# Performance work log

Hardware: AMD Instinct MI355X
Metric: run time of the kernel (lower is better)

The kernel has to match this reference:

```python
import jax, jax.numpy as jnp
import numpy as np

N, IN_C, HID, H1, E, EP = 4096, 256, 128, 4, 131072, 131072
TH, TL, FF = 4, 2, 512  # transformer heads, layers, ffn dim
D = HID  # transformer d_model


def setup_inputs() -> dict:
    key = jax.random.key(0)
    ks = jax.random.split(key, 32)
    s = 0.05
    inp = {
        'features': jax.random.normal(ks[0], (N, IN_C), jnp.float32),
        'src': jax.random.randint(ks[1], (E,), 0, N),
        'dst': jax.random.randint(ks[2], (E,), 0, N),
        'psrc': jax.random.randint(ks[3], (EP,), 0, N),
        'pdst': jax.random.randint(ks[4], (EP,), 0, N),
        # GAT layer 1: in=256 -> heads=4, out=128
        'W1': jax.random.normal(ks[5], (H1 * HID, IN_C), jnp.float32) * s,
        'al1': jax.random.normal(ks[6], (H1, HID), jnp.float32) * s,
        'ar1': jax.random.normal(ks[7], (H1, HID), jnp.float32) * s,
        'b1': jnp.zeros((H1 * HID,), jnp.float32),
        # GAT layer 2: in=512 -> heads=1, out=128
        'W2': jax.random.normal(ks[8], (HID, H1 * HID), jnp.float32) * s,
        'al2': jax.random.normal(ks[9], (1, HID), jnp.float32) * s,
        'ar2': jax.random.normal(ks[10], (1, HID), jnp.float32) * s,
        'b2': jnp.zeros((HID,), jnp.float32),
        # Transformer encoder (TL layers, torch TransformerEncoderLayer post-norm, relu)
        'tw_qkv': jax.random.normal(ks[11], (TL, 3 * D, D), jnp.float32) * s,
        'tb_qkv': jnp.zeros((TL, 3 * D), jnp.float32),
        'tw_o': jax.random.normal(ks[12], (TL, D, D), jnp.float32) * s,
        'tb_o': jnp.zeros((TL, D), jnp.float32),
        'ln1_g': jnp.ones((TL, D), jnp.float32),
        'ln1_b': jnp.zeros((TL, D), jnp.float32),
        'tw_ff1': jax.random.normal(ks[13], (TL, FF, D), jnp.float32) * s,
        'tb_ff1': jnp.zeros((TL, FF), jnp.float32),
        'tw_ff2': jax.random.normal(ks[14], (TL, D, FF), jnp.float32) * s,
        'tb_ff2': jnp.zeros((TL, D), jnp.float32),
        'ln2_g': jnp.ones((TL, D), jnp.float32),
        'ln2_b': jnp.zeros((TL, D), jnp.float32),
        # decoder MLP
        'fc1_w': jax.random.normal(ks[15], (HID, 2 * HID), jnp.float32) * s,
        'fc1_b': jnp.zeros((HID,), jnp.float32),
        'fc2_w': jax.random.normal(ks[16], (1, HID), jnp.float32) * s,
        'fc2_b': jnp.zeros((1,), jnp.float32),
    }
    return inp


def _leaky(x):
    return jnp.where(x > 0, x, 0.2 * x)


def _gat(x, W, al, ar, b, src, dst, n):
    H, F = al.shape
    h = (x @ W.T).reshape(n, H, F)  # [N,H,F]
    el = jnp.sum(h * al[None], -1)  # [N,H]
    er = jnp.sum(h * ar[None], -1)
    e = _leaky(el[src] + er[dst])  # [E,H]
    m = jax.ops.segment_max(e, dst, num_segments=n)
    ex = jnp.exp(e - m[dst])
    ssum = jax.ops.segment_sum(ex, dst, num_segments=n)
    alpha = ex / ssum[dst]  # edge softmax over incoming edges of dst
    out = jax.ops.segment_sum(h[src] * alpha[:, :, None], dst, num_segments=n)
    return out + b.reshape(1, H, F)


def _ln(x, g, b):
    mu = jnp.mean(x, -1, keepdims=True)
    var = jnp.mean((x - mu) ** 2, -1, keepdims=True)
    return (x - mu) / jnp.sqrt(var + 1e-5) * g + b


def _encoder_layer(h, wqkv, bqkv, wo, bo, g1, b1, wf1, bf1, wf2, bf2, g2, b2):
    n, d = h.shape
    hd = d // TH
    qkv = h @ wqkv.T + bqkv
    q, k, v = jnp.split(qkv, 3, axis=-1)
    q = q.reshape(n, TH, hd)
    k = k.reshape(n, TH, hd)
    v = v.reshape(n, TH, hd)
    scores = jnp.einsum('qhd,khd->hqk', q, k) / jnp.sqrt(jnp.float32(hd))
    attn = jax.nn.softmax(scores, axis=-1)
    o = jnp.einsum('hqk,khd->qhd', attn, v).reshape(n, d) @ wo.T + bo
    h = _ln(h + o, g1, b1)
    ff = jax.nn.relu(h @ wf1.T + bf1) @ wf2.T + bf2
    return _ln(h + ff, g2, b2)


def reference(features, W1, al1, ar1, b1, W2, al2, ar2, b2,
              tw_qkv, tb_qkv, tw_o, tb_o, ln1_g, ln1_b,
              tw_ff1, tb_ff1, tw_ff2, tb_ff2, ln2_g, ln2_b,
              fc1_w, fc1_b, fc2_w, fc2_b, src, dst, psrc, pdst):
    n = features.shape[0]
    h = _gat(features, W1, al1, ar1, b1, src, dst, n)  # [N,4,128]
    h = jax.nn.relu(h.reshape(n, -1))                  # [N,512]
    h = _gat(h, W2, al2, ar2, b2, src, dst, n)[:, 0]   # [N,128]
    for i in range(TL):
        h = _encoder_layer(h, tw_qkv[i], tb_qkv[i], tw_o[i], tb_o[i],
                           ln1_g[i], ln1_b[i], tw_ff1[i], tb_ff1[i],
                           tw_ff2[i], tb_ff2[i], ln2_g[i], ln2_b[i])
    ef = jnp.concatenate([h[psrc], h[pdst]], axis=1)   # [EP,256]
    x = jax.nn.relu(ef @ fc1_w.T + fc1_b)
    return jax.nn.sigmoid(x @ fc2_w.T + fc2_b)         # [EP,1]
```

## Files before the change

kernel.cpp:

```cpp
#include <hip/hip_runtime.h>
#include <hip/hip_bf16.h>
#include <math.h>

#define NN   4096
#define INC  256
#define HIDF 128
#define H1H  4
#define DM   128
#define THD  4
#define FFD  512

typedef __attribute__((ext_vector_type(8))) short bf16x8;
typedef __attribute__((ext_vector_type(4))) float f32x4;

__device__ __forceinline__ float leaky(float x){ return x > 0.f ? x : 0.2f*x; }

__device__ __forceinline__ ushort f2b(float f){
  __hip_bfloat16 h = __float2bfloat16(f);
  return __builtin_bit_cast(ushort, h);
}
__device__ __forceinline__ unsigned pk2(float a, float b){
  return (unsigned)f2b(a) | ((unsigned)f2b(b) << 16);
}
__device__ __forceinline__ float b2f(unsigned u){ return __uint_as_float(u << 16); }
__device__ __forceinline__ float b2flo(unsigned u){ return __uint_as_float(u << 16); }
__device__ __forceinline__ float b2fhi(unsigned u){ return __uint_as_float(u & 0xffff0000u); }

__device__ __forceinline__ int kvperm(int kv){
  return (kv & ~31) | ((kv & 12) << 1) | ((kv >> 2) & 4) | (kv & 3);
}

template<bool BIAS, bool RELU, bool OUTBF, bool ABF>
__global__ __launch_bounds__(256) void gemm_mf(
    const void* __restrict__ Av, const ushort* __restrict__ Wb,
    const float* __restrict__ bias, void* __restrict__ Cv,
    int M, int N, int K, int ldw)
{
  __shared__ uint4 As4[512];
  __shared__ uint4 Bs4[512];
  int tid = threadIdx.x;
  int row0 = blockIdx.y * 64, col0 = blockIdx.x * 64;
  int wid = tid >> 6, lane = tid & 63;
  int wm = wid >> 1, wn = wid & 1;
  int ql = lane & 15, g = lane >> 4;
  const f32x4 z4 = {0.f,0.f,0.f,0.f};
  f32x4 acc[2][2] = {z4,z4,z4,z4};

  for (int k0 = 0; k0 < K; k0 += 64) {
    #pragma unroll
    for (int p = 0; p < 2; p++) {
      int idx = tid + p*256;
      int ko = idx & 7, mm = idx >> 3;
      if constexpr (ABF) {
        As4[ko*64 + mm] = *(const uint4*)((const ushort*)Av + (size_t)(row0 + mm)*K + k0 + ko*8);
      } else {
        const float* sa = (const float*)Av + (size_t)(row0 + mm)*K + k0 + ko*8;
        float4 a0 = *(const float4*)sa;
        float4 a1 = *(const float4*)(sa + 4);
        uint4 av;
        av.x = pk2(a0.x, a0.y); av.y = pk2(a0.z, a0.w);
        av.z = pk2(a1.x, a1.y); av.w = pk2(a1.z, a1.w);
        As4[ko*64 + mm] = av;
      }
      Bs4[ko*64 + mm] = *(const uint4*)(Wb + (size_t)(col0 + mm)*ldw + k0 + ko*8);
    }
    __syncthreads();
    #pragma unroll
    for (int kk = 0; kk < 2; kk++) {
      int ko = kk*4 + g;
      bf16x8 a0 = *((const bf16x8*)As4 + ko*64 + wm*32 + ql);
      bf16x8 a1 = *((const bf16x8*)As4 + ko*64 + wm*32 + 16 + ql);
      bf16x8 b0 = *((const bf16x8*)Bs4 + ko*64 + wn*32 + ql);
      bf16x8 b1 = *((const bf16x8*)Bs4 + ko*64 + wn*32 + 16 + ql);
      acc[0][0] = __builtin_amdgcn_mfma_f32_16x16x32_bf16(a0, b0, acc[0][0], 0,0,0);
      acc[0][1] = __builtin_amdgcn_mfma_f32_16x16x32_bf16(a0, b1, acc[0][1], 0,0,0);
      acc[1][0] = __builtin_amdgcn_mfma_f32_16x16x32_bf16(a1, b0, acc[1][0], 0,0,0);
      acc[1][1] = __builtin_amdgcn_mfma_f32_16x16x32_bf16(a1, b1, acc[1][1], 0,0,0);
    }
    __syncthreads();
  }
  float bvs[2] = {0.f, 0.f};
  if (BIAS) {
    bvs[0] = bias[col0 + wn*32 + ql];
    bvs[1] = bias[col0 + wn*32 + 16 + ql];
  }
  #pragma unroll
  for (int fm = 0; fm < 2; fm++)
    #pragma unroll
    for (int fn = 0; fn < 2; fn++) {
      int row = row0 + wm*32 + fm*16 + g*4;
      int col = col0 + wn*32 + fn*16 + ql;
      #pragma unroll
      for (int r = 0; r < 4; r++) {
        float v = acc[fm][fn][r];
        if (BIAS) v += bvs[fn];
        if (RELU) v = fmaxf(v, 0.f);
        if (OUTBF) ((ushort*)Cv)[(size_t)(row + r)*N + col] = f2b(v);
        else       ((float*)Cv)[(size_t)(row + r)*N + col] = v;
      }
    }
}

__global__ __launch_bounds__(256) void gemm_qkv(
    const ushort* __restrict__ Ab, const ushort* __restrict__ Wb,
    const float* __restrict__ bias,
    ushort* __restrict__ qb, ushort* __restrict__ kt, ushort* __restrict__ vt)
{
  __shared__ uint4 As4[512];
  __shared__ uint4 Bs4[512];
  int tid = threadIdx.x;
  int row0 = blockIdx.y * 64, col0 = blockIdx.x * 64;
  int wid = tid >> 6, lane = tid & 63;
  int wm = wid >> 1, wn = wid & 1;
  int ql = lane & 15, g = lane >> 4;
  const f32x4 z4 = {0.f,0.f,0.f,0.f};
  f32x4 acc[2][2] = {z4,z4,z4,z4};

  for (int k0 = 0; k0 < 128; k0 += 64) {
    #pragma unroll
    for (int p = 0; p < 2; p++) {
      int idx = tid + p*256;
      int ko = idx & 7, mm = idx >> 3;
      As4[ko*64 + mm] = *(const uint4*)(Ab + (size_t)(row0 + mm)*128 + k0 + ko*8);
      Bs4[ko*64 + mm] = *(const uint4*)(Wb + (size_t)(col0 + mm)*128 + k0 + ko*8);
    }
    __syncthreads();
    #pragma unroll
    for (int kk = 0; kk < 2; kk++) {
      int ko = kk*4 + g;
      bf16x8 a0 = *((const bf16x8*)As4 + ko*64 + wm*32 + ql);
      bf16x8 a1 = *((const bf16x8*)As4 + ko*64 + wm*32 + 16 + ql);
      bf16x8 b0 = *((const bf16x8*)Bs4 + ko*64 + wn*32 + ql);
      bf16x8 b1 = *((const bf16x8*)Bs4 + ko*64 + wn*32 + 16 + ql);
      acc[0][0] = __builtin_amdgcn_mfma_f32_16x16x32_bf16(a0, b0, acc[0][0], 0,0,0);
      acc[0][1] = __builtin_amdgcn_mfma_f32_16x16x32_bf16(a0, b1, acc[0][1], 0,0,0);
      acc[1][0] = __builtin_amdgcn_mfma_f32_16x16x32_bf16(a1, b0, acc[1][0], 0,0,0);
      acc[1][1] = __builtin_amdgcn_mfma_f32_16x16x32_bf16(a1, b1, acc[1][1], 0,0,0);
    }
    __syncthreads();
  }
  float bvs[2];
  bvs[0] = bias[col0 + wn*32 + ql];
  bvs[1] = bias[col0 + wn*32 + 16 + ql];
  #pragma unroll
  for (int fm = 0; fm < 2; fm++)
    #pragma unroll
    for (int fn = 0; fn < 2; fn++) {
      int row = row0 + wm*32 + fm*16 + g*4;
      int col = col0 + wn*32 + fn*16 + ql;
      #pragma unroll
      for (int r = 0; r < 4; r++) {
        float v = acc[fm][fn][r] + bvs[fn];
        int kv = row + r;
        if (col < 128) {
          qb[(size_t)kv*128 + col] = f2b(v * 0.25505654708f);
        } else if (col < 256) {
          int hh = (col - 128) >> 5, d = (col - 128) & 31;
          kt[(size_t)hh*131072 + (size_t)kv*32 + d] = f2b(v);
        } else {
          int hh = (col - 256) >> 5, d = (col - 256) & 31;
          vt[(size_t)hh*131072 + (size_t)(kv >> 5)*1024 + (d >> 4)*512
             + (d & 15)*32 + kvperm(kv & 31)] = f2b(v);
        }
      }
    }
}

__global__ __launch_bounds__(256) void gemm_ln(
    const ushort* __restrict__ Ab, const ushort* __restrict__ Wb,
    const float* __restrict__ bias, ushort* __restrict__ h,
    const float* __restrict__ lng, const float* __restrict__ lnb, int K)
{
  __shared__ uint4 As4[128];
  __shared__ uint4 Bs4[1024];
  __shared__ float xs[16][132];
  int tid = threadIdx.x;
  int row0 = blockIdx.x * 16;
  int wv = tid >> 6, lane = tid & 63;
  int ql = lane & 15, g = lane >> 4;
  const f32x4 z4 = {0.f,0.f,0.f,0.f};
  f32x4 acc[2] = {z4, z4};

  for (int k0 = 0; k0 < K; k0 += 64) {
    if (tid < 128) {
      int ko = tid & 7, mm = tid >> 3;
      As4[ko*16 + mm] = *(const uint4*)(Ab + (size_t)(row0 + mm)*K + k0 + ko*8);
    }
    #pragma unroll
    for (int p = 0; p < 4; p++) {
      int idx = tid + p*256;
      int ko = idx & 7, nn = idx >> 3;
      Bs4[ko*128 + nn] = *(const uint4*)(Wb + (size_t)nn*K + k0 + ko*8);
    }
    __syncthreads();
    #pragma unroll
    for (int kk = 0; kk < 2; kk++) {
      int ko = kk*4 + g;
      bf16x8 a = *((const bf16x8*)As4 + ko*16 + ql);
      #pragma unroll
      for (int fn = 0; fn < 2; fn++) {
        bf16x8 b = *((const bf16x8*)Bs4 + ko*128 + wv*32 + fn*16 + ql);
        acc[fn] = __builtin_amdgcn_mfma_f32_16x16x32_bf16(a, b, acc[fn], 0,0,0);
      }
    }
    __syncthreads();
  }
  #pragma unroll
  for (int fn = 0; fn < 2; fn++) {
    int col = wv*32 + fn*16 + ql;
    float bv = bias[col];
    #pragma unroll
    for (int r = 0; r < 4; r++) xs[g*4 + r][col] = acc[fn][r] + bv;
  }
  __syncthreads();
  int rl = tid >> 4, cl = tid & 15, c0 = cl * 8;
  ushort* hrow = h + (size_t)(row0 + rl)*128;
  uint4 rv = *(const uint4*)(hrow + c0);
  float x[8];
  x[0] = xs[rl][c0+0] + b2flo(rv.x); x[1] = xs[rl][c0+1] + b2fhi(rv.x);
  x[2] = xs[rl][c0+2] + b2flo(rv.y); x[3] = xs[rl][c0+3] + b2fhi(rv.y);
  x[4] = xs[rl][c0+4] + b2flo(rv.z); x[5] = xs[rl][c0+5] + b2fhi(rv.z);
  x[6] = xs[rl][c0+6] + b2flo(rv.w); x[7] = xs[rl][c0+7] + b2fhi(rv.w);
  float s1 = 0.f, s2 = 0.f;
  #pragma unroll
  for (int i = 0; i < 8; i++) { s1 += x[i]; s2 += x[i]*x[i]; }
  #pragma unroll
  for (int st = 1; st < 16; st <<= 1) {
    s1 += __shfl_xor(s1, st); s2 += __shfl_xor(s2, st);
  }
  float mean = s1 * (1.f/128.f);
  float var  = s2 * (1.f/128.f) - mean*mean;
  float rstd = rsqrtf(var + 1e-5f);
  float o[8];
  #pragma unroll
  for (int i = 0; i < 8; i += 4) {
    float4 g4 = *(const float4*)(lng + c0 + i);
    float4 b4 = *(const float4*)(lnb + c0 + i);
    o[i+0] = (x[i+0]-mean)*rstd*g4.x + b4.x;
    o[i+1] = (x[i+1]-mean)*rstd*g4.y + b4.y;
    o[i+2] = (x[i+2]-mean)*rstd*g4.z + b4.z;
    o[i+3] = (x[i+3]-mean)*rstd*g4.w + b4.w;
  }
  uint4 ov; ov.x = pk2(o[0],o[1]); ov.y = pk2(o[2],o[3]);
  ov.z = pk2(o[4],o[5]); ov.w = pk2(o[6],o[7]);
  *(uint4*)(hrow + c0) = ov;
}

__global__ __launch_bounds__(256) void cvt_weights(
    const float* __restrict__ W1, const float* __restrict__ W2,
    const float* __restrict__ qkv, const float* __restrict__ o,
    const float* __restrict__ ff1, const float* __restrict__ ff2,
    const float* __restrict__ fc1, const float* __restrict__ fc1b,
    ushort* __restrict__ out, float* __restrict__ bias256)
{
  if (blockIdx.x == 608) {
    int t = threadIdx.x;
    bias256[t] = (t < 128) ? fc1b[t] : 0.f;
    return;
  }
  int i4 = (blockIdx.x*256 + threadIdx.x) * 4;
  const float* s; int loc;
  size_t dst = i4;
  if      (i4 < 131072) { s = W1;  loc = i4; }
  else if (i4 < 196608) { s = W2;  loc = i4 - 131072; }
  else if (i4 < 294912) { s = qkv; loc = i4 - 196608; }
  else if (i4 < 327680) { s = o;   loc = i4 - 294912; }
  else if (i4 < 458752) { s = ff1; loc = i4 - 327680; }
  else if (i4 < 589824) { s = ff2; loc = i4 - 458752; }
  else {
    s = fc1; loc = i4 - 589824;
    int j = loc >> 8, k2 = loc & 255;
    dst = 589824 + ((k2 >= 128) ? 16384 : 0) + j*128 + (k2 & 127);
  }
  float4 v = *(const float4*)(s + loc);
  uint2 w; w.x = pk2(v.x, v.y); w.y = pk2(v.z, v.w);
  *(uint2*)(out + dst) = w;
}

__global__ void zero_kernel(int* p, int n) {
  int i = blockIdx.x * blockDim.x + threadIdx.x;
  if (i < n) p[i] = 0;
}
__global__ void count_kernel(const int* __restrict__ dst, int* __restrict__ deg, int E) {
  int e = blockIdx.x * blockDim.x + threadIdx.x;
  if (e < E) atomicAdd(&deg[dst[e]], 1);
}
__global__ __launch_bounds__(1024) void scan_kernel(
    const int* __restrict__ deg, int* __restrict__ rowstart, int* __restrict__ cursor)
{
  __shared__ int sdata[1024];
  int t = threadIdx.x;
  int base = t * 4;
  int v0 = deg[base], v1 = deg[base+1], v2 = deg[base+2], v3 = deg[base+3];
  int tot = v0 + v1 + v2 + v3;
  sdata[t] = tot;
  __syncthreads();
  for (int off = 1; off < 1024; off <<= 1) {
    int x = (t >= off) ? sdata[t - off] : 0;
    __syncthreads();
    sdata[t] += x;
    __syncthreads();
  }
  int run = sdata[t] - tot;
  rowstart[base]   = run; cursor[base]   = run; run += v0;
  rowstart[base+1] = run; cursor[base+1] = run; run += v1;
  rowstart[base+2] = run; cursor[base+2] = run; run += v2;
  rowstart[base+3] = run; cursor[base+3] = run; run += v3;
  if (t == 1023) rowstart[4096] = run;
}
__global__ void fill_kernel(const int* __restrict__ src, const int* __restrict__ dst,
                            int* __restrict__ cursor, int* __restrict__ nbr, int E) {
  int e = blockIdx.x * blockDim.x + threadIdx.x;
  if (e < E) {
    int p = atomicAdd(&cursor[dst[e]], 1);
    nbr[p] = src[e];
  }
}

template<int H>
__global__ __launch_bounds__(256) void elr_kernel(
    const ushort* __restrict__ hmat, const float* __restrict__ al,
    const float* __restrict__ ar, float* __restrict__ el, float* __restrict__ er)
{
  int w = threadIdx.x >> 6, lane = threadIdx.x & 63;
  int n = blockIdx.x * 4 + w;
  if constexpr (H == 4) {
    int hh = lane >> 4, f0 = (lane & 15) * 8;
    bf16x8 hv = *(const bf16x8*)(hmat + (size_t)n*512 + hh*128 + f0);
    float4 a0 = *(const float4*)(al + hh*128 + f0);
    float4 a1 = *(const float4*)(al + hh*128 + f0 + 4);
    float4 r0 = *(const float4*)(ar + hh*128 + f0);
    float4 r1 = *(const float4*)(ar + hh*128 + f0 + 4);
    float x[8];
    #pragma unroll
    for (int i = 0; i < 8; i++) x[i] = b2f((ushort)hv[i]);
    float e1 = x[0]*a0.x + x[1]*a0.y + x[2]*a0.z + x[3]*a0.w
             + x[4]*a1.x + x[5]*a1.y + x[6]*a1.z + x[7]*a1.w;
    float e2 = x[0]*r0.x + x[1]*r0.y + x[2]*r0.z + x[3]*r0.w
             + x[4]*r1.x + x[5]*r1.y + x[6]*r1.z + x[7]*r1.w;
    #pragma unroll
    for (int s = 1; s < 16; s <<= 1) { e1 += __shfl_xor(e1, s); e2 += __shfl_xor(e2, s); }
    if ((lane & 15) == 0) { el[n*4 + hh] = e1; er[n*4 + hh] = e2; }
  } else {
    int f0 = lane * 2;
    unsigned u = *(const unsigned*)(hmat + (size_t)n*128 + f0);
    float x0 = b2flo(u), x1 = b2fhi(u);
    float2 av = *(const float2*)(al + f0);
    float2 rv = *(const float2*)(ar + f0);
    float e1 = x0*av.x + x1*av.y;
    float e2 = x0*rv.x + x1*rv.y;
    #pragma unroll
    for (int s = 1; s < 64; s <<= 1) { e1 += __shfl_xor(e1, s); e2 += __shfl_xor(e2, s); }
    if (lane == 0) { el[n] = e1; er[n] = e2; }
  }
}

__global__ __launch_bounds__(256) void gat_agg4(
    const ushort* __restrict__ hsrc, const float* __restrict__ el, const float* __restrict__ er,
    const int* __restrict__ rowstart, const int* __restrict__ nbr,
    const float* __restrict__ bias, ushort* __restrict__ out)
{
  __shared__ float s_alpha[4][256][4];
  __shared__ int   s_nbr[4][256];
  int wv = threadIdx.x >> 6, lane = threadIdx.x & 63;
  int n = blockIdx.x * 4 + wv;
  int e0 = rowstart[n];
  int deg = rowstart[n+1] - e0;
  float4 ern = *(const float4*)(er + (size_t)n*4);
  int hh = lane >> 4;
  float acc[8] = {};
  if (deg > 0 && deg <= 256) {
    float se0=0.f, se1=0.f, se2=0.f, se3=0.f;
    for (int i = lane; i < deg; i += 64) {
      int s = nbr[e0 + i];
      s_nbr[wv][i] = s;
      float4 ev = *(const float4*)(el + (size_t)s*4);
      float p0 = __expf(leaky(ev.x + ern.x));
      float p1 = __expf(leaky(ev.y + ern.y));
      float p2 = __expf(leaky(ev.z + ern.z));
      float p3 = __expf(leaky(ev.w + ern.w));
      s_alpha[wv][i][0] = p0; s_alpha[wv][i][1] = p1;
      s_alpha[wv][i][2] = p2; s_alpha[wv][i][3] = p3;
      se0 += p0; se1 += p1; se2 += p2; se3 += p3;
    }
    #pragma unroll
    for (int st = 1; st < 64; st <<= 1) {
      se0 += __shfl_xor(se0, st); se1 += __shfl_xor(se1, st);
      se2 += __shfl_xor(se2, st); se3 += __shfl_xor(se3, st);
    }
    float si = 1.f / ((hh == 0) ? se0 : (hh == 1) ? se1 : (hh == 2) ? se2 : se3);
    #pragma unroll 4
    for (int i = 0; i < deg; i++) {
      float a = s_alpha[wv][i][hh] * si;
      int s = s_nbr[wv][i];
      uint4 hv = *(const uint4*)(hsrc + (size_t)s*512 + lane*8);
      acc[0] += a * b2flo(hv.x); acc[1] += a * b2fhi(hv.x);
      acc[2] += a * b2flo(hv.y); acc[3] += a * b2fhi(hv.y);
      acc[4] += a * b2flo(hv.z); acc[5] += a * b2fhi(hv.z);
      acc[6] += a * b2flo(hv.w); acc[7] += a * b2fhi(hv.w);
    }
  } else if (deg > 0) {
    float se0=0.f, se1=0.f, se2=0.f, se3=0.f;
    for (int i = lane; i < deg; i += 64) {
      int s = nbr[e0 + i];
      float4 ev = *(const float4*)(el + (size_t)s*4);
      se0 += __expf(leaky(ev.x + ern.x));
      se1 += __expf(leaky(ev.y + ern.y));
      se2 += __expf(leaky(ev.z + ern.z));
      se3 += __expf(leaky(ev.w + ern.w));
    }
    #pragma unroll
    for (int st = 1; st < 64; st <<= 1) {
      se0 += __shfl_xor(se0, st); se1 += __shfl_xor(se1, st);
      se2 += __shfl_xor(se2, st); se3 += __shfl_xor(se3, st);
    }
    float si0 = 1.f/se0, si1 = 1.f/se1, si2 = 1.f/se2, si3 = 1.f/se3;
    for (int c = 0; c < deg; c += 256) {
      int cn = min(256, deg - c);
      for (int i = lane; i < cn; i += 64) {
        int s = nbr[e0 + c + i];
        s_nbr[wv][i] = s;
        float4 ev = *(const float4*)(el + (size_t)s*4);
        s_alpha[wv][i][0] = __expf(leaky(ev.x + ern.x)) * si0;
        s_alpha[wv][i][1] = __expf(leaky(ev.y + ern.y)) * si1;
        s_alpha[wv][i][2] = __expf(leaky(ev.z + ern.z)) * si2;
        s_alpha[wv][i][3] = __expf(leaky(ev.w + ern.w)) * si3;
      }
      #pragma unroll 4
      for (int i = 0; i < cn; i++) {
        float a = s_alpha[wv][i][hh];
        int s = s_nbr[wv][i];
        uint4 hv = *(const uint4*)(hsrc + (size_t)s*512 + lane*8);
        acc[0] += a * b2flo(hv.x); acc[1] += a * b2fhi(hv.x);
        acc[2] += a * b2flo(hv.y); acc[3] += a * b2fhi(hv.y);
        acc[4] += a * b2flo(hv.z); acc[5] += a * b2fhi(hv.z);
        acc[6] += a * b2flo(hv.w); acc[7] += a * b2fhi(hv.w);
      }
    }
  }
  const float* bp = bias + lane*8;
  float4 b0 = *(const float4*)(bp);
  float4 b1 = *(const float4*)(bp + 4);
  float v0 = fmaxf(acc[0]+b0.x, 0.f), v1 = fmaxf(acc[1]+b0.y, 0.f);
  float v2 = fmaxf(acc[2]+b0.z, 0.f), v3 = fmaxf(acc[3]+b0.w, 0.f);
  float v4 = fmaxf(acc[4]+b1.x, 0.f), v5 = fmaxf(acc[5]+b1.y, 0.f);
  float v6 = fmaxf(acc[6]+b1.z, 0.f), v7 = fmaxf(acc[7]+b1.w, 0.f);
  uint4 ov; ov.x = pk2(v0,v1); ov.y = pk2(v2,v3); ov.z = pk2(v4,v5); ov.w = pk2(v6,v7);
  *(uint4*)(out + (size_t)n*512 + lane*8) = ov;
}

__global__ __launch_bounds__(256) void gat_agg1(
    const ushort* __restrict__ hsrc, const float* __restrict__ el, const float* __restrict__ er,
    const int* __restrict__ rowstart, const int* __restrict__ nbr,
    const float* __restrict__ bias, ushort* __restrict__ out)
{
  __shared__ float s_alpha[4][256];
  __shared__ int   s_nbr[4][256];
  int wv = threadIdx.x >> 6, lane = threadIdx.x & 63;
  int n = blockIdx.x * 4 + wv;
  int e0 = rowstart[n];
  int deg = rowstart[n+1] - e0;
  float ern = er[n];
  float a0 = 0.f, a1 = 0.f;
  if (deg > 0 && deg <= 256) {
    float se = 0.f;
    for (int i = lane; i < deg; i += 64) {
      int s = nbr[e0 + i];
      s_nbr[wv][i] = s;
      float p = __expf(leaky(el[s] + ern));
      s_alpha[wv][i] = p;
      se += p;
    }
    #pragma unroll
    for (int st = 1; st < 64; st <<= 1) se += __shfl_xor(se, st);
    float si = 1.f / se;
    #pragma unroll 4
    for (int i = 0; i < deg; i++) {
      float a = s_alpha[wv][i] * si;
      int s = s_nbr[wv][i];
      unsigned u = *(const unsigned*)(hsrc + (size_t)s*128 + lane*2);
      a0 += a * b2flo(u);
      a1 += a * b2fhi(u);
    }
  } else if (deg > 0) {
    float se = 0.f;
    for (int i = lane; i < deg; i += 64)
      se += __expf(leaky(el[nbr[e0 + i]] + ern));
    #pragma unroll
    for (int st = 1; st < 64; st <<= 1) se += __shfl_xor(se, st);
    float si = 1.f / se;
    for (int c = 0; c < deg; c += 256) {
      int cn = min(256, deg - c);
      for (int i = lane; i < cn; i += 64) {
        int s = nbr[e0 + c + i];
        s_nbr[wv][i] = s;
        s_alpha[wv][i] = __expf(leaky(el[s] + ern)) * si;
      }
      #pragma unroll 4
      for (int i = 0; i < cn; i++) {
        float a = s_alpha[wv][i];
        int s = s_nbr[wv][i];
        unsigned u = *(const unsigned*)(hsrc + (size_t)s*128 + lane*2);
        a0 += a * b2flo(u);
        a1 += a * b2fhi(u);
      }
    }
    a0 *= si; a1 *= si;
    a0 /= si; a1 /= si;
  }
  float v0 = a0 + bias[lane*2], v1 = a1 + bias[lane*2 + 1];
  *(unsigned*)(out + (size_t)n*128 + lane*2) = pk2(v0, v1);
}

#define LOADFRAGS(KF, VF, KV)                                              \
  {                                                                        \
    int _kv = (KV);                                                        \
    if (_kv < 1024) {                                                      \
      const ushort* _kp = kptr + (size_t)_kv * 32;                         \
      const ushort* _vp = vptr + (size_t)_kv * 32;                         \
      KF[0] = *(const bf16x8*)(_kp);                                       \
      KF[1] = *(const bf16x8*)(_kp + 512);                                 \
      KF[2] = *(const bf16x8*)(_kp + 1024);                                \
      KF[3] = *(const bf16x8*)(_kp + 1536);                                \
      VF[0] = *(const bf16x8*)(_vp);                                       \
      VF[1] = *(const bf16x8*)(_vp + 1024);                                \
      VF[2] = *(const bf16x8*)(_vp + 512);                                 \
      VF[3] = *(const bf16x8*)(_vp + 1536);                                \
    }                                                                      \
  }

#define QPASS(QF, LS, OA, OB, KF, VF)                                      \
  {                                                                        \
    f32x4 st0 = __builtin_amdgcn_mfma_f32_16x16x32_bf16(KF[0], QF, z4, 0, 0, 0); \
    f32x4 st1 = __builtin_amdgcn_mfma_f32_16x16x32_bf16(KF[1], QF, z4, 0, 0, 0); \
    f32x4 st2 = __builtin_amdgcn_mfma_f32_16x16x32_bf16(KF[2], QF, z4, 0, 0, 0); \
    f32x4 st3 = __builtin_amdgcn_mfma_f32_16x16x32_bf16(KF[3], QF, z4, 0, 0, 0); \
    float pvv[16];                                                         \
    _Pragma("unroll")                                                      \
    for (int i = 0; i < 4; i++) {                                          \
      pvv[i] = st0[i]; pvv[4+i] = st1[i]; pvv[8+i] = st2[i]; pvv[12+i] = st3[i]; \
    }                                                                      \
    _Pragma("unroll")                                                      \
    for (int i = 0; i < 16; i++) { pvv[i] = exp2f(pvv[i]); LS += pvv[i]; } \
    bf16x8 pf0 = { (short)f2b(pvv[0]),  (short)f2b(pvv[1]),  (short)f2b(pvv[2]),  (short)f2b(pvv[3]),   \
                   (short)f2b(pvv[4]),  (short)f2b(pvv[5]),  (short)f2b(pvv[6]),  (short)f2b(pvv[7]) }; \
    bf16x8 pf1 = { (short)f2b(pvv[8]),  (short)f2b(pvv[9]),  (short)f2b(pvv[10]), (short)f2b(pvv[11]),  \
                   (short)f2b(pvv[12]), (short)f2b(pvv[13]), (short)f2b(pvv[14]), (short)f2b(pvv[15]) };\
    OA = __builtin_amdgcn_mfma_f32_16x16x32_bf16(VF[0], pf0, OA, 0, 0, 0); \
    OA = __builtin_amdgcn_mfma_f32_16x16x32_bf16(VF[1], pf1, OA, 0, 0, 0); \
    OB = __builtin_amdgcn_mfma_f32_16x16x32_bf16(VF[2], pf0, OB, 0, 0, 0); \
    OB = __builtin_amdgcn_mfma_f32_16x16x32_bf16(VF[3], pf1, OB, 0, 0, 0); \
  }

#define ATTN_BODY(KF, VF, KN, VN, KV)                                      \
  {                                                                        \
    LOADFRAGS(KN, VN, (KV) + 64);                                          \
    QPASS(qf0, ls0, o00, o01, KF, VF);                                     \
    QPASS(qf1, ls1, o10, o11, KF, VF);                                     \
  }

__global__ __launch_bounds__(256) void attn_mfma(
    const ushort* __restrict__ qb,
    const ushort* __restrict__ kt,
    const ushort* __restrict__ vt,
    ushort* __restrict__ attnout)
{
  int lane = threadIdx.x & 63;
  int w    = threadIdx.x >> 6;
  int head = blockIdx.x >> 7;
  int q0   = (blockIdx.x & 127) * 32;
  int ql = lane & 15;
  int g  = lane >> 4;
  const f32x4 z4 = {0.f, 0.f, 0.f, 0.f};
  int kvbase = w * 1024;

  bf16x8 qf0 = *(const bf16x8*)(qb + (size_t)(q0 + ql)*128      + head*32 + g*8);
  bf16x8 qf1 = *(const bf16x8*)(qb + (size_t)(q0 + 16 + ql)*128 + head*32 + g*8);
  const ushort* kptr = kt + (size_t)head*131072 + (size_t)kvbase*32 + ql*32 + g*8;
  const ushort* vptr = vt + (size_t)head*131072 + (size_t)kvbase*32 + ql*32 + g*8;

  float ls0 = 0.f, ls1 = 0.f;
  f32x4 o00 = z4, o01 = z4, o10 = z4, o11 = z4;

  bf16x8 kfA[4], vfA[4], kfB[4], vfB[4];
  LOADFRAGS(kfA, vfA, 0);
  for (int kv0 = 0; kv0 < 1024; kv0 += 128) {
    ATTN_BODY(kfA, vfA, kfB, vfB, kv0);
    ATTN_BODY(kfB, vfB, kfA, vfA, kv0 + 64);
  }

  ls0 += __shfl_xor(ls0, 16); ls0 += __shfl_xor(ls0, 32);
  ls1 += __shfl_xor(ls1, 16); ls1 += __shfl_xor(ls1, 32);

  __shared__ float so[4][32][36];
  __shared__ float sl[4][32];
  if (g == 0) { sl[w][ql] = ls0; sl[w][16 + ql] = ls1; }
  #pragma unroll
  for (int r = 0; r < 4; r++) {
    so[w][ql][g*4 + r]           = o00[r];
    so[w][ql][16 + g*4 + r]      = o01[r];
    so[w][16 + ql][g*4 + r]      = o10[r];
    so[w][16 + ql][16 + g*4 + r] = o11[r];
  }
  __syncthreads();
  int q  = threadIdx.x >> 3;
  int d0 = (threadIdx.x & 7) * 4;
  float L = 0.f, O0 = 0.f, O1 = 0.f, O2 = 0.f, O3 = 0.f;
  #pragma unroll
  for (int w2 = 0; w2 < 4; w2++) {
    L  += sl[w2][q];
    O0 += so[w2][q][d0];
    O1 += so[w2][q][d0+1];
    O2 += so[w2][q][d0+2];
    O3 += so[w2][q][d0+3];
  }
  float rl = 1.f / L;
  uint2 w2v; w2v.x = pk2(O0*rl, O1*rl); w2v.y = pk2(O2*rl, O3*rl);
  *(uint2*)(attnout + (size_t)(q0 + q)*128 + head*32 + d0) = w2v;
}

__global__ __launch_bounds__(256) void pair_kernel(
    const ushort* __restrict__ ABp,
    const int* __restrict__ ps, const int* __restrict__ pd,
    const float* __restrict__ fc2w, const float* __restrict__ fc2b,
    float* __restrict__ out, int EP)
{
  int gw = (blockIdx.x * blockDim.x + threadIdx.x) >> 6;
  int lane = threadIdx.x & 63;
  int nw = (gridDim.x * blockDim.x) >> 6;
  float w0 = fc2w[2*lane], w1 = fc2w[2*lane + 1];
  float bb = fc2b[0];
  for (int p = gw; p < EP; p += nw) {
    int s = ps[p], d = pd[p];
    unsigned av = *(const unsigned*)(ABp + (size_t)s*256 + 2*lane);
    unsigned bv = *(const unsigned*)(ABp + (size_t)d*256 + 128 + 2*lane);
    float a0 = b2flo(av), a1 = b2fhi(av);
    float b0 = b2flo(bv), b1 = b2fhi(bv);
    float acc = fmaxf(a0 + b0, 0.f)*w0 + fmaxf(a1 + b1, 0.f)*w1;
    #pragma unroll
    for (int off = 32; off > 0; off >>= 1) acc += __shfl_down(acc, off);
    if (lane == 0) out[p] = 1.f / (1.f + __expf(-(acc + bb)));
  }
}

extern "C" void kernel_launch(void* const* d_in, const int* in_sizes, int n_in,
                              void* d_out, int out_size, void* d_ws, size_t ws_size,
                              hipStream_t stream)
{
  const float* features = (const float*)d_in[0];
  const int*   src      = (const int*)d_in[1];
  const int*   dst      = (const int*)d_in[2];
  const int*   psrc     = (const int*)d_in[3];
  const int*   pdst     = (const int*)d_in[4];
  const float* W1   = (const float*)d_in[5];
  const float* al1  = (const float*)d_in[6];
  const float* ar1  = (const float*)d_in[7];
  const float* b1   = (const float*)d_in[8];
  const float* W2   = (const float*)d_in[9];
  const float* al2  = (const float*)d_in[10];
  const float* ar2  = (const float*)d_in[11];
  const float* b2   = (const float*)d_in[12];
  const float* tw_qkv = (const float*)d_in[13];
  const float* tb_qkv = (const float*)d_in[14];
  const float* tw_o   = (const float*)d_in[15];
  const float* tb_o   = (const float*)d_in[16];
  const float* ln1_g  = (const float*)d_in[17];
  const float* ln1_b  = (const float*)d_in[18];
  const float* tw_ff1 = (const float*)d_in[19];
  const float* tb_ff1 = (const float*)d_in[20];
  const float* tw_ff2 = (const float*)d_in[21];
  const float* tb_ff2 = (const float*)d_in[22];
  const float* ln2_g  = (const float*)d_in[23];
  const float* ln2_b  = (const float*)d_in[24];
  const float* fc1_w  = (const float*)d_in[25];
  const float* fc1_b  = (const float*)d_in[26];
  const float* fc2_w  = (const float*)d_in[27];
  const float* fc2_b  = (const float*)d_in[28];
  int E  = in_sizes[1];
  int EP = in_sizes[3];

  float* ws = (float*)d_ws;
  size_t off = 0;
  auto alloc = [&](size_t n) { float* p = ws + off; off += n; return p; };
  ushort* hb    = (ushort*)alloc((size_t)NN * 64);
  ushort* h1b   = (ushort*)alloc((size_t)NN * 256);
  ushort* h2b   = (ushort*)alloc((size_t)NN * 256);
  ushort* bigb  = (ushort*)alloc((size_t)NN * 256);
  ushort* hgb   = (ushort*)alloc((size_t)NN * 64);
  ushort* qb    = (ushort*)alloc((size_t)NN * 64);
  ushort* attnb = (ushort*)alloc((size_t)NN * 64);
  ushort* kt    = (ushort*)alloc((size_t)NN * 64);
  ushort* vt    = (ushort*)alloc((size_t)NN * 64);
  ushort* wbf   = (ushort*)alloc(622592/2);
  ushort* ABp   = (ushort*)alloc((size_t)NN * 128);
  float*  bias256 = alloc(256);
  float*  el1   = alloc((size_t)NN * 4);
  float*  er1   = alloc((size_t)NN * 4);
  float*  el2   = alloc((size_t)NN);
  float*  er2   = alloc((size_t)NN);
  int* ibase    = (int*)(ws + off);
  int* deg      = ibase;
  int* rowstart = ibase + 4096;
  int* cursor   = rowstart + 4097;
  int* nbr      = cursor + 4096;

  const size_t oW1 = 0, oW2 = 131072, oQKV = 196608, oO = 294912,
               oFF1 = 327680, oFF2 = 458752, oFC1 = 589824;

  cvt_weights<<<609, 256, 0, stream>>>(W1, W2, tw_qkv, tw_o, tw_ff1, tw_ff2,
                                       fc1_w, fc1_b, wbf, bias256);

  zero_kernel<<<16, 256, 0, stream>>>(deg, 4096);
  count_kernel<<<(E + 255)/256, 256, 0, stream>>>(dst, deg, E);
  scan_kernel<<<1, 1024, 0, stream>>>(deg, rowstart, cursor);
  fill_kernel<<<(E + 255)/256, 256, 0, stream>>>(src, dst, cursor, nbr, E);

  gemm_mf<false,false,true,false><<<dim3(8, 64), 256, 0, stream>>>(
      features, wbf + oW1, nullptr, h1b, NN, 512, 256, 256);
  elr_kernel<4><<<1024, 256, 0, stream>>>(h1b, al1, ar1, el1, er1);
  gat_agg4<<<1024, 256, 0, stream>>>(h1b, el1, er1, rowstart, nbr, b1, h2b);

  gemm_mf<false,false,true,true><<<dim3(2, 64), 256, 0, stream>>>(
      h2b, wbf + oW2, nullptr, hgb, NN, 128, 512, 512);
  elr_kernel<1><<<1024, 256, 0, stream>>>(hgb, al2, ar2, el2, er2);
  gat_agg1<<<1024, 256, 0, stream>>>(hgb, el2, er2, rowstart, nbr, b2, hb);

  for (int l = 0; l < 2; l++) {
    gemm_qkv<<<dim3(6, 64), 256, 0, stream>>>(
        hb, wbf + oQKV + (size_t)l*49152, tb_qkv + l*384, qb, kt, vt);
    attn_mfma<<<512, 256, 0, stream>>>(qb, kt, vt, attnb);
    gemm_ln<<<256, 256, 0, stream>>>(
        attnb, wbf + oO + (size_t)l*16384, tb_o + l*128, hb,
        ln1_g + l*128, ln1_b + l*128, 128);
    gemm_mf<true,true,true,true><<<dim3(8, 64), 256, 0, stream>>>(
        hb, wbf + oFF1 + (size_t)l*65536, tb_ff1 + l*512, bigb, NN, 512, 128, 128);
    gemm_ln<<<256, 256, 0, stream>>>(
        bigb, wbf + oFF2 + (size_t)l*65536, tb_ff2 + l*128, hb,
        ln2_g + l*128, ln2_b + l*128, 512);
  }

  gemm_mf<true,false,true,true><<<dim3(4, 64), 256, 0, stream>>>(
      hb, wbf + oFC1, bias256, ABp, NN, 256, 128, 128);
  pair_kernel<<<1024, 256, 0, stream>>>(ABp, psrc, pdst, fc2_w, fc2_b, (float*)d_out, EP);
}
```

Before: 218.8 us.

## Split attention KV across 8 waves, pre-convert features, batch pair pairs, memset degrees

The attention kernel now runs 512 threads per block, and each of 8 waves covers 512 keys instead of 4 waves covering 1024. This raises parallelism per block at the cost of a larger shared-memory reduction. Input features are converted to bf16 in a separate kernel so the first GEMM reads bf16 instead of fp32. The pair kernel processes two edges per wave iteration to overlap gathers. A redundant multiply/divide in gat_agg1 is removed, and the zero kernel is replaced with hipMemsetAsync.

```diff
diff --git a/kernel.cpp b/kernel.cpp
--- a/kernel.cpp
+++ b/kernel.cpp
@@ -277,10 +277,15 @@
   *(uint2*)(out + dst) = w;
 }
 
-__global__ void zero_kernel(int* p, int n) {
-  int i = blockIdx.x * blockDim.x + threadIdx.x;
-  if (i < n) p[i] = 0;
-}
+__global__ __launch_bounds__(256) void cvt_feat(
+    const float* __restrict__ f, ushort* __restrict__ o)
+{
+  int i = (blockIdx.x * 256 + threadIdx.x) * 4;
+  float4 v = *(const float4*)(f + i);
+  uint2 w; w.x = pk2(v.x, v.y); w.y = pk2(v.z, v.w);
+  *(uint2*)(o + i) = w;
+}
+
 __global__ void count_kernel(const int* __restrict__ dst, int* __restrict__ deg, int E) {
   int e = blockIdx.x * blockDim.x + threadIdx.x;
   if (e < E) atomicAdd(&deg[dst[e]], 1);
@@ -505,8 +510,6 @@
         a1 += a * b2fhi(u);
       }
     }
-    a0 *= si; a1 *= si;
-    a0 /= si; a1 /= si;
   }
   float v0 = a0 + bias[lane*2], v1 = a1 + bias[lane*2 + 1];
   *(unsigned*)(out + (size_t)n*128 + lane*2) = pk2(v0, v1);
@@ -515,7 +518,7 @@
 #define LOADFRAGS(KF, VF, KV)                                              \
   {                                                                        \
     int _kv = (KV);                                                        \
-    if (_kv < 1024) {                                                      \
+    if (_kv < 512) {                                                       \
       const ushort* _kp = kptr + (size_t)_kv * 32;                         \
       const ushort* _vp = vptr + (size_t)_kv * 32;                         \
       KF[0] = *(const bf16x8*)(_kp);                                       \
@@ -559,7 +562,7 @@
     QPASS(qf1, ls1, o10, o11, KF, VF);                                     \
   }
 
-__global__ __launch_bounds__(256) void attn_mfma(
+__global__ __launch_bounds__(512) void attn_mfma(
     const ushort* __restrict__ qb,
     const ushort* __restrict__ kt,
     const ushort* __restrict__ vt,
@@ -572,7 +575,7 @@
   int ql = lane & 15;
   int g  = lane >> 4;
   const f32x4 z4 = {0.f, 0.f, 0.f, 0.f};
-  int kvbase = w * 1024;
+  int kvbase = w * 512;
 
   bf16x8 qf0 = *(const bf16x8*)(qb + (size_t)(q0 + ql)*128      + head*32 + g*8);
   bf16x8 qf1 = *(const bf16x8*)(qb + (size_t)(q0 + 16 + ql)*128 + head*32 + g*8);
@@ -584,7 +587,7 @@
 
   bf16x8 kfA[4], vfA[4], kfB[4], vfB[4];
   LOADFRAGS(kfA, vfA, 0);
-  for (int kv0 = 0; kv0 < 1024; kv0 += 128) {
+  for (int kv0 = 0; kv0 < 512; kv0 += 128) {
     ATTN_BODY(kfA, vfA, kfB, vfB, kv0);
     ATTN_BODY(kfB, vfB, kfA, vfA, kv0 + 64);
   }
@@ -592,8 +595,8 @@
   ls0 += __shfl_xor(ls0, 16); ls0 += __shfl_xor(ls0, 32);
   ls1 += __shfl_xor(ls1, 16); ls1 += __shfl_xor(ls1, 32);
 
-  __shared__ float so[4][32][36];
-  __shared__ float sl[4][32];
+  __shared__ float so[8][32][36];
+  __shared__ float sl[8][32];
   if (g == 0) { sl[w][ql] = ls0; sl[w][16 + ql] = ls1; }
   #pragma unroll
   for (int r = 0; r < 4; r++) {
@@ -603,20 +606,17 @@
     so[w][16 + ql][16 + g*4 + r] = o11[r];
   }
   __syncthreads();
-  int q  = threadIdx.x >> 3;
-  int d0 = (threadIdx.x & 7) * 4;
-  float L = 0.f, O0 = 0.f, O1 = 0.f, O2 = 0.f, O3 = 0.f;
+  int q  = threadIdx.x >> 4;
+  int d0 = (threadIdx.x & 15) * 2;
+  float L = 0.f, O0 = 0.f, O1 = 0.f;
   #pragma unroll
-  for (int w2 = 0; w2 < 4; w2++) {
+  for (int w2 = 0; w2 < 8; w2++) {
     L  += sl[w2][q];
     O0 += so[w2][q][d0];
     O1 += so[w2][q][d0+1];
-    O2 += so[w2][q][d0+2];
-    O3 += so[w2][q][d0+3];
   }
   float rl = 1.f / L;
-  uint2 w2v; w2v.x = pk2(O0*rl, O1*rl); w2v.y = pk2(O2*rl, O3*rl);
-  *(uint2*)(attnout + (size_t)(q0 + q)*128 + head*32 + d0) = w2v;
+  *(unsigned*)(attnout + (size_t)(q0 + q)*128 + head*32 + d0) = pk2(O0*rl, O1*rl);
 }
 
 __global__ __launch_bounds__(256) void pair_kernel(
@@ -630,16 +630,28 @@
   int nw = (gridDim.x * blockDim.x) >> 6;
   float w0 = fc2w[2*lane], w1 = fc2w[2*lane + 1];
   float bb = fc2b[0];
-  for (int p = gw; p < EP; p += nw) {
-    int s = ps[p], d = pd[p];
-    unsigned av = *(const unsigned*)(ABp + (size_t)s*256 + 2*lane);
-    unsigned bv = *(const unsigned*)(ABp + (size_t)d*256 + 128 + 2*lane);
-    float a0 = b2flo(av), a1 = b2fhi(av);
-    float b0 = b2flo(bv), b1 = b2fhi(bv);
-    float acc = fmaxf(a0 + b0, 0.f)*w0 + fmaxf(a1 + b1, 0.f)*w1;
-    #pragma unroll
-    for (int off = 32; off > 0; off >>= 1) acc += __shfl_down(acc, off);
-    if (lane == 0) out[p] = 1.f / (1.f + __expf(-(acc + bb)));
+  for (int p = gw*2; p < EP; p += nw*2) {
+    int sA = ps[p], dA = pd[p];
+    bool hasB = (p + 1 < EP);
+    int sB = hasB ? ps[p+1] : sA;
+    int dB = hasB ? pd[p+1] : dA;
+    unsigned avA = *(const unsigned*)(ABp + (size_t)sA*256 + 2*lane);
+    unsigned bvA = *(const unsigned*)(ABp + (size_t)dA*256 + 128 + 2*lane);
+    unsigned avB = *(const unsigned*)(ABp + (size_t)sB*256 + 2*lane);
+    unsigned bvB = *(const unsigned*)(ABp + (size_t)dB*256 + 128 + 2*lane);
+    float accA = fmaxf(b2flo(avA) + b2flo(bvA), 0.f)*w0
+               + fmaxf(b2fhi(avA) + b2fhi(bvA), 0.f)*w1;
+    float accB = fmaxf(b2flo(avB) + b2flo(bvB), 0.f)*w0
+               + fmaxf(b2fhi(avB) + b2fhi(bvB), 0.f)*w1;
+    #pragma unroll
+    for (int off = 32; off > 0; off >>= 1) {
+      accA += __shfl_down(accA, off);
+      accB += __shfl_down(accB, off);
+    }
+    if (lane == 0) {
+      out[p] = 1.f / (1.f + __expf(-(accA + bb)));
+      if (hasB) out[p+1] = 1.f / (1.f + __expf(-(accB + bb)));
+    }
   }
 }
 
@@ -683,6 +695,7 @@
   size_t off = 0;
   auto alloc = [&](size_t n) { float* p = ws + off; off += n; return p; };
   ushort* hb    = (ushort*)alloc((size_t)NN * 64);
+  ushort* featb = (ushort*)alloc((size_t)NN * 128);
   ushort* h1b   = (ushort*)alloc((size_t)NN * 256);
   ushort* h2b   = (ushort*)alloc((size_t)NN * 256);
   ushort* bigb  = (ushort*)alloc((size_t)NN * 256);
@@ -709,14 +722,15 @@
 
   cvt_weights<<<609, 256, 0, stream>>>(W1, W2, tw_qkv, tw_o, tw_ff1, tw_ff2,
                                        fc1_w, fc1_b, wbf, bias256);
-
-  zero_kernel<<<16, 256, 0, stream>>>(deg, 4096);
+  cvt_feat<<<1024, 256, 0, stream>>>(features, featb);
+
+  hipMemsetAsync(deg, 0, 4096 * sizeof(int), stream);
   count_kernel<<<(E + 255)/256, 256, 0, stream>>>(dst, deg, E);
   scan_kernel<<<1, 1024, 0, stream>>>(deg, rowstart, cursor);
   fill_kernel<<<(E + 255)/256, 256, 0, stream>>>(src, dst, cursor, nbr, E);
 
-  gemm_mf<false,false,true,false><<<dim3(8, 64), 256, 0, stream>>>(
-      features, wbf + oW1, nullptr, h1b, NN, 512, 256, 256);
+  gemm_mf<false,false,true,true><<<dim3(8, 64), 256, 0, stream>>>(
+      featb, wbf + oW1, nullptr, h1b, NN, 512, 256, 256);
   elr_kernel<4><<<1024, 256, 0, stream>>>(h1b, al1, ar1, el1, er1);
   gat_agg4<<<1024, 256, 0, stream>>>(h1b, el1, er1, rowstart, nbr, b1, h2b);
 
@@ -728,7 +742,7 @@
   for (int l = 0; l < 2; l++) {
     gemm_qkv<<<dim3(6, 64), 256, 0, stream>>>(
         hb, wbf + oQKV + (size_t)l*49152, tb_qkv + l*384, qb, kt, vt);
-    attn_mfma<<<512, 256, 0, stream>>>(qb, kt, vt, attnb);
+    attn_mfma<<<512, 512, 0, stream>>>(qb, kt, vt, attnb);
     gemm_ln<<<256, 256, 0, stream>>>(
         attnb, wbf + oO + (size_t)l*16384, tb_o + l*128, hb,
         ln1_g + l*128, ln1_b + l*128, 128);
```

After: 212.4 us. -2.9%, faster.
